# Kernel tuning notes

Measured on AMD Instinct MI355X. Metric: run time of the kernel, lower is better.

## Reference

```python
import jax, jax.numpy as jnp
import numpy as np

B, T, W = 8, 4096, 1024          # batch, byte seq len, words per sequence
DB, DW = 64, 512                 # byte_embed_dim, word_embed_dim
NH = 2                           # highway layers per block
VOCAB = 264                      # 256 bytes + 4 + 4 specials
BPE_MARK, WORD_MARK = 4, 3       # bpe_mask_idx, word_mask_idx


def _make_seg_ids():
    # ragged word lengths in {3,4,5}, mean 4, summing to T per sequence
    rng = np.random.default_rng(0)
    seg = np.empty((B, T), np.int32)
    base = T // W
    for b in range(B):
        delta = np.zeros(W, np.int64)
        q = W // 4
        idx = rng.permutation(W)
        delta[idx[:q]] = 1
        delta[idx[q:2 * q]] = -1
        seg[b] = np.repeat(np.arange(W), base + delta)
    return jnp.asarray(seg)


def setup_inputs() -> dict:
    key = jax.random.key(0)
    ks = jax.random.split(key, 12)
    s = 0.05
    byte_tokens = jax.random.randint(ks[0], (B, T), 4, VOCAB)
    bpe_mask = jax.random.bernoulli(ks[1], 0.25, (B, T))
    word_mask = jax.random.bernoulli(ks[2], 0.05, (B, T))
    seg_ids = _make_seg_ids()
    tok_emb = (jax.random.normal(ks[3], (VOCAB, DB)) * s).at[0].set(0.0)  # padding_idx=0 row zeroed
    inp = {
        'byte_tokens': byte_tokens, 'bpe_mask': bpe_mask, 'word_mask': word_mask,
        'seg_ids': seg_ids, 'tok_emb': tok_emb,
        'conv0_w': jax.random.normal(ks[4], (3, DB, DW)) * s, 'conv0_b': jnp.zeros((DW,)),
        'hw0_wg': jax.random.normal(ks[5], (NH, DW, DW)) * s, 'hw0_bg': jnp.zeros((NH, DW)),
        'hw0_wh': jax.random.normal(ks[6], (NH, DW, DW)) * s, 'hw0_bh': jnp.zeros((NH, DW)),
        'conv1_w': jax.random.normal(ks[7], (3, DW, DW)) * s, 'conv1_b': jnp.zeros((DW,)),
        'hw1_wg': jax.random.normal(ks[8], (NH, DW, DW)) * s, 'hw1_bg': jnp.zeros((NH, DW)),
        'hw1_wh': jax.random.normal(ks[9], (NH, DW, DW)) * s, 'hw1_bh': jnp.zeros((NH, DW)),
        'proj_w': jax.random.normal(ks[10], (DW, DW)) * s, 'proj_b': jnp.zeros((DW,)),
    }
    return inp


def _conv_highway(x, cw, cb, wg, bg, wh, bh, residual):
    # 1D same-padded conv over sequence, optional residual, relu, then highways
    y = jax.lax.conv_general_dilated(x, cw, (1,), 'SAME',
                                     dimension_numbers=('NWC', 'WIO', 'NWC')) + cb
    if residual:
        y = y + x
    y = jax.nn.relu(y)
    for i in range(NH):
        g = jax.nn.sigmoid(y @ wg[i] + bg[i])
        h = jax.nn.relu(y @ wh[i] + bh[i])
        y = g * h + (1.0 - g) * y
    return y


def reference(byte_tokens, bpe_mask, word_mask, seg_ids, tok_emb,
              conv0_w, conv0_b, hw0_wg, hw0_bg, hw0_wh, hw0_bh,
              conv1_w, conv1_b, hw1_wg, hw1_bg, hw1_wh, hw1_bh,
              proj_w, proj_b):
    # byte embedding + marker embeddings (pad idx 0 -> zero row)
    x = (tok_emb[byte_tokens]
         + tok_emb[jnp.where(bpe_mask, BPE_MARK, 0)]
         + tok_emb[jnp.where(word_mask, WORD_MARK, 0)])          # [B,T,DB]
    x = _conv_highway(x, conv0_w, conv0_b, hw0_wg, hw0_bg, hw0_wh, hw0_bh, False)
    x = _conv_highway(x, conv1_w, conv1_b, hw1_wg, hw1_bg, hw1_wh, hw1_bh, True)
    # ragged per-word segment max over bytes (fused, replaces python loops)
    seg_max = jax.vmap(lambda xi, si: jax.ops.segment_max(xi, si, num_segments=W))
    x = seg_max(x, seg_ids)                                       # [B,W,DW]
    return x @ proj_w + proj_b
```

## Files before the change

### kernel.cpp

```cpp
#include <hip/hip_runtime.h>
#include <hip/hip_bf16.h>

using bf16 = __hip_bfloat16;
typedef __attribute__((ext_vector_type(8))) short s8v;
typedef __attribute__((ext_vector_type(4))) float f4v;

#define T_SEQ 4096
#define DWC 512

__device__ __forceinline__ float fin(float v) {
    return (v == v && fabsf(v) < 1e30f) ? v : 0.0f;
}
__device__ __forceinline__ float ldf(const void* p, size_t i, int f32) {
    return f32 ? ((const float*)p)[i] : __bfloat162float(((const bf16*)p)[i]);
}
__device__ __forceinline__ float b2f(short s) {
    unsigned u = ((unsigned)(unsigned short)s) << 16;
    return __builtin_bit_cast(float, u);
}
__device__ __forceinline__ short f2b(float v) {
    bf16 b = __float2bfloat16(v);
    return __builtin_bit_cast(short, b);
}
__device__ __forceinline__ uint4 ld16(const short* p) { return *(const uint4*)p; }

__device__ __forceinline__ void swz(int L, int G, int& bx, int& by) {
    int k8 = L & 7, sl = L >> 3;
    int gp = G >> 5;
    bx = sl & 3;
    by = k8 * gp + (sl >> 2);
}

__device__ __forceinline__ int swidx(int row, int ch) {
    return row * 32 + ((ch ^ ((row >> 1) & 3)) << 3);
}

__global__ __launch_bounds__(256) void diag_kernel(bf16* __restrict__ out, int n, float v)
{
    int i = blockIdx.x * 256 + threadIdx.x;
    if (i < n) out[i] = __float2bfloat16(i == 0 ? v : 0.0f);
}

__global__ __launch_bounds__(256) void detect_kernel(
    const int* __restrict__ tok, const unsigned char* __restrict__ bpe,
    const unsigned char* __restrict__ wm, const int* __restrict__ seg,
    const unsigned int* __restrict__ embw, int* __restrict__ flags)
{
    __shared__ int sh[5];
    int tid = threadIdx.x;
    if (tid < 5) sh[tid] = 0;
    __syncthreads();
    int bo = 0, bm = 0, wo = 0, wmid = 0;
    for (int i = tid; i < 16384; i += 256) {
        int odd = 2 * i + 1;
        if (bpe[odd]) bo = 1;
        if (wm[odd])  wo = 1;
        int mid = 8 * (i & 4095) + 4;
        if (bpe[mid]) bm = 1;
        if (wm[mid])  wmid = 1;
    }
    if (bo)   atomicOr(&sh[0], 1);
    if (bm)   atomicOr(&sh[1], 1);
    if (wo)   atomicOr(&sh[2], 1);
    if (wmid) atomicOr(&sh[3], 1);
    if (tid < 32 && embw[32 + tid] != 0u) atomicOr(&sh[4], 1);
    __syncthreads();
    if (tid == 0) {
        flags[0] = (tok[32767] != 0) ? 0 : 1;
        flags[1] = sh[0] ? 1 : (sh[1] ? 4 : 8);
        flags[2] = sh[2] ? 1 : (sh[3] ? 4 : 8);
        flags[3] = (seg[32767] != 0) ? 0 : 1;
        flags[4] = sh[4] ? 0 : 1;
    }
}

#define WB_TOTAL 3249664
#define EMB4_ELEMS (264 * 4 * 64)
__global__ __launch_bounds__(256) void convert_weights(
    const void* c0w, const void* c0b, const void* h0g, const void* h0bg,
    const void* h0h, const void* h0bh, const void* c1w, const void* c1b,
    const void* h1g, const void* h1bg, const void* h1h, const void* h1bh,
    const void* pw, const void* pb, const void* emb,
    const int* __restrict__ flags, short* __restrict__ WB)
{
    int f32 = flags[4];
    size_t i = (size_t)blockIdx.x * 256 + threadIdx.x;
    if (i >= WB_TOTAL + EMB4_ELEMS) return;
    if (i >= WB_TOTAL) {
        size_t o = i - WB_TOTAL;
        size_t t = o >> 8, v = (o >> 6) & 3, c = o & 63;
        float val = ldf(emb, t * 64 + c, f32);
        if (v & 1) val += ldf(emb, 4 * 64 + c, f32);
        if (v & 2) val += ldf(emb, 3 * 64 + c, f32);
        WB[i] = f2b(fin(val));
        return;
    }
    const void* src; size_t si;
    if (i < 98304)        { size_t n = i / 192, k = i % 192; src = c0w; si = k * 512 + n; }
    else if (i < 98816)   { src = c0b;  si = i - 98304; }
    else if (i < 623104)  { size_t o = i - 98816;  size_t l = o >> 18; o &= 262143;
                            size_t n = o >> 9, k = o & 511; src = h0g; si = (l << 18) + k * 512 + n; }
    else if (i < 624128)  { src = h0bg; si = i - 623104; }
    else if (i < 1148416) { size_t o = i - 624128; size_t l = o >> 18; o &= 262143;
                            size_t n = o >> 9, k = o & 511; src = h0h; si = (l << 18) + k * 512 + n; }
    else if (i < 1149440) { src = h0bh; si = i - 1148416; }
    else if (i < 1935872) { size_t o = i - 1149440; size_t n = o / 1536, k = o % 1536;
                            src = c1w; si = k * 512 + n; }
    else if (i < 1936384) { src = c1b;  si = i - 1935872; }
    else if (i < 2460672) { size_t o = i - 1936384; size_t l = o >> 18; o &= 262143;
                            size_t n = o >> 9, k = o & 511; src = h1g; si = (l << 18) + k * 512 + n; }
    else if (i < 2461696) { src = h1bg; si = i - 2460672; }
    else if (i < 2985984) { size_t o = i - 2461696; size_t l = o >> 18; o &= 262143;
                            size_t n = o >> 9, k = o & 511; src = h1h; si = (l << 18) + k * 512 + n; }
    else if (i < 2987008) { src = h1bh; si = i - 2985984; }
    else if (i < 3249152) { size_t o = i - 2987008; size_t n = o >> 9, k = o & 511;
                            src = pw; si = k * 512 + n; }
    else                  { src = pb;   si = i - 3249152; }
    WB[i] = f2b(ldf(src, si, f32));
}

__global__ __launch_bounds__(512) void conv0_mfma(
    const int* __restrict__ tok, const unsigned char* __restrict__ bpe,
    const unsigned char* __restrict__ wm, const short* __restrict__ emb4,
    const int* __restrict__ flags, const short* __restrict__ WT,
    const short* __restrict__ bias, short* __restrict__ Out)
{
    constexpr int K = 192;
    constexpr int NIT = 3;
    __shared__ __align__(16) short As[2][256 * 32];
    __shared__ __align__(16) short Bs[2][256 * 32];
    int bx, by;
    swz(blockIdx.x, gridDim.x, bx, by);
    const int bm = by * 128, bn = bx * 128;
    const int tid = threadIdx.x;
    const int wave = tid >> 6, lane = tid & 63;
    const int wmr = (wave >> 1) * 32, wnc = (wave & 1) * 64;
    const int q = lane >> 4, ln16 = lane & 15;
    const int sr = tid >> 2, sch = tid & 3;
    const int tt = (bm + sr) & (T_SEQ - 1);
    const int is64t = flags[0];
    const int wb = flags[1], ww = flags[2];
    const short* Bb = WT + (size_t)(bn + sr) * K + sch * 8;

    f4v acc[2][4] = {};
    uint4 rA0, rA1, rB0, rB1;
    const uint4 z4 = make_uint4(0, 0, 0, 0);

    auto loadA = [&](int tap, uint4& a0, uint4& a1) {
        int ts = tt + tap - 1;
        if ((unsigned)ts < (unsigned)T_SEQ) {
            int bt = bm + sr + tap - 1;
            int tk = is64t ? (int)((const long long*)tok)[bt] : tok[bt];
            tk = min(max(tk, 0), 263);
            int v = (bpe[(size_t)bt * wb] ? 1 : 0) | (wm[(size_t)bt * ww] ? 2 : 0);
            const short* row = emb4 + ((size_t)tk * 4 + v) * 64;
            a0 = ld16(row + sch * 8);
            a1 = ld16(row + 32 + sch * 8);
        } else { a0 = z4; a1 = z4; }
    };

    loadA(0, rA0, rA1);
    rB0 = ld16(Bb);
    rB1 = ld16(Bb + 32);
    *(uint4*)(&As[0][swidx(sr, sch)])       = rA0;
    *(uint4*)(&As[0][swidx(128 + sr, sch)]) = rA1;
    *(uint4*)(&Bs[0][swidx(sr, sch)])       = rB0;
    *(uint4*)(&Bs[0][swidx(128 + sr, sch)]) = rB1;
    __syncthreads();
    int p = 0;

    for (int it = 0; it < NIT; ++it) {
        const bool more = (it + 1 < NIT);
        if (more) {
            int kn = (it + 1) * 64;
            loadA(it + 1, rA0, rA1);
            rB0 = ld16(Bb + kn);
            rB1 = ld16(Bb + kn + 32);
        }
        #pragma unroll
        for (int ks = 0; ks < 2; ks++) {
            s8v af[2], bf[4];
            #pragma unroll
            for (int mi = 0; mi < 2; mi++)
                af[mi] = *(const s8v*)(&As[p][swidx(128 * ks + wmr + mi * 16 + ln16, q)]);
            #pragma unroll
            for (int ni = 0; ni < 4; ni++)
                bf[ni] = *(const s8v*)(&Bs[p][swidx(128 * ks + wnc + ni * 16 + ln16, q)]);
            #pragma unroll
            for (int mi = 0; mi < 2; mi++)
                #pragma unroll
                for (int ni = 0; ni < 4; ni++)
                    acc[mi][ni] = __builtin_amdgcn_mfma_f32_16x16x32_bf16(
                        af[mi], bf[ni], acc[mi][ni], 0, 0, 0);
        }
        if (more) {
            *(uint4*)(&As[p ^ 1][swidx(sr, sch)])       = rA0;
            *(uint4*)(&As[p ^ 1][swidx(128 + sr, sch)]) = rA1;
            *(uint4*)(&Bs[p ^ 1][swidx(sr, sch)])       = rB0;
            *(uint4*)(&Bs[p ^ 1][swidx(128 + sr, sch)]) = rB1;
            __syncthreads();
            p ^= 1;
        }
    }

    #pragma unroll
    for (int mi = 0; mi < 2; mi++)
        #pragma unroll
        for (int ni = 0; ni < 4; ni++) {
            int col = bn + wnc + ni * 16 + ln16;
            float bv = b2f(bias[col]);
            #pragma unroll
            for (int r = 0; r < 4; r++) {
                int orow = bm + wmr + mi * 16 + q * 4 + r;
                Out[(size_t)orow * DWC + col] =
                    f2b(fin(fmaxf(acc[mi][ni][r] + bv, 0.0f)));
            }
        }
}

__global__ __launch_bounds__(512) void conv1_mfma(
    const short* __restrict__ A, const short* __restrict__ WT,
    const short* __restrict__ bias, short* __restrict__ Out)
{
    constexpr int IC = 512;
    constexpr int K = 3 * IC;
    constexpr int NIT = K / 64;
    __shared__ __align__(16) short As[2][256 * 32];
    __shared__ __align__(16) short Bs[2][256 * 32];
    int bx, by;
    swz(blockIdx.x, gridDim.x, bx, by);
    const int bm = by * 128, bn = bx * 128;
    const int tid = threadIdx.x;
    const int wave = tid >> 6, lane = tid & 63;
    const int wmr = (wave >> 1) * 32, wnc = (wave & 1) * 64;
    const int q = lane >> 4, ln16 = lane & 15;
    const int sr = tid >> 2, sch = tid & 3;
    const int tt = (bm + sr) & (T_SEQ - 1);
    const short* Bb = WT + (size_t)(bn + sr) * K + sch * 8;

    f4v acc[2][4] = {};
    uint4 rA0, rA1, rB0, rB1;
    const uint4 z4 = make_uint4(0, 0, 0, 0);

    {
        int ts = tt - 1;
        bool ok = (ts >= 0 && ts < T_SEQ);
        const short* sa = A + (size_t)(bm + sr - 1) * IC + sch * 8;
        rA0 = ok ? ld16(sa) : z4;
        rA1 = ok ? ld16(sa + 32) : z4;
        rB0 = ld16(Bb);
        rB1 = ld16(Bb + 32);
    }
    *(uint4*)(&As[0][swidx(sr, sch)])       = rA0;
    *(uint4*)(&As[0][swidx(128 + sr, sch)]) = rA1;
    *(uint4*)(&Bs[0][swidx(sr, sch)])       = rB0;
    *(uint4*)(&Bs[0][swidx(128 + sr, sch)]) = rB1;
    __syncthreads();
    int p = 0;

    for (int it = 0; it < NIT; ++it) {
        const bool more = (it + 1 < NIT);
        if (more) {
            int kn = (it + 1) * 64;
            int tap = kn / IC, c0 = kn - tap * IC;
            int ts = tt + tap - 1;
            bool ok = (ts >= 0 && ts < T_SEQ);
            const short* sa = A + (size_t)(bm + sr + tap - 1) * IC + c0 + sch * 8;
            rA0 = ok ? ld16(sa) : z4;
            rA1 = ok ? ld16(sa + 32) : z4;
            rB0 = ld16(Bb + kn);
            rB1 = ld16(Bb + kn + 32);
        }
        #pragma unroll
        for (int ks = 0; ks < 2; ks++) {
            s8v af[2], bf[4];
            #pragma unroll
            for (int mi = 0; mi < 2; mi++)
                af[mi] = *(const s8v*)(&As[p][swidx(128 * ks + wmr + mi * 16 + ln16, q)]);
            #pragma unroll
            for (int ni = 0; ni < 4; ni++)
                bf[ni] = *(const s8v*)(&Bs[p][swidx(128 * ks + wnc + ni * 16 + ln16, q)]);
            #pragma unroll
            for (int mi = 0; mi < 2; mi++)
                #pragma unroll
                for (int ni = 0; ni < 4; ni++)
                    acc[mi][ni] = __builtin_amdgcn_mfma_f32_16x16x32_bf16(
                        af[mi], bf[ni], acc[mi][ni], 0, 0, 0);
        }
        if (more) {
            *(uint4*)(&As[p ^ 1][swidx(sr, sch)])       = rA0;
            *(uint4*)(&As[p ^ 1][swidx(128 + sr, sch)]) = rA1;
            *(uint4*)(&Bs[p ^ 1][swidx(sr, sch)])       = rB0;
            *(uint4*)(&Bs[p ^ 1][swidx(128 + sr, sch)]) = rB1;
            __syncthreads();
            p ^= 1;
        }
    }

    #pragma unroll
    for (int mi = 0; mi < 2; mi++)
        #pragma unroll
        for (int ni = 0; ni < 4; ni++) {
            int col = bn + wnc + ni * 16 + ln16;
            float bv = b2f(bias[col]);
            #pragma unroll
            for (int r = 0; r < 4; r++) {
                int orow = bm + wmr + mi * 16 + q * 4 + r;
                float v = acc[mi][ni][r] + bv + b2f(A[(size_t)orow * IC + col]);
                Out[(size_t)orow * DWC + col] = f2b(fin(fmaxf(v, 0.0f)));
            }
        }
}

__global__ __launch_bounds__(512) void highway_mfma8(
    const short* __restrict__ Y, const short* __restrict__ WgT,
    const short* __restrict__ bg, const short* __restrict__ WhT,
    const short* __restrict__ bh, short* __restrict__ Out)
{
    constexpr int IC = DWC;
    constexpr int NIT = IC / 64;
    __shared__ __align__(16) short As [2][512 * 32];
    __shared__ __align__(16) short Bgs[2][256 * 32];
    __shared__ __align__(16) short Bhs[2][256 * 32];
    int bx, by;
    swz(blockIdx.x, gridDim.x, bx, by);
    const int bm = by * 256, bn = bx * 128;
    const int tid = threadIdx.x;
    const int wave = tid >> 6, lane = tid & 63;
    const int wmr = (wave >> 2) * 128;
    const int wnc = (wave & 3) * 32;
    const int q = lane >> 4, ln16 = lane & 15;
    const int sr = tid >> 2, sch = tid & 3;

    const short* A0 = Y   + (size_t)(bm + sr) * IC + sch * 8;
    const short* A1 = A0 + 128 * IC;
    const short* G0 = WgT + (size_t)(bn + sr) * IC + sch * 8;
    const short* H0 = WhT + (size_t)(bn + sr) * IC + sch * 8;

    f4v accg[8][2] = {};
    f4v acch[8][2] = {};
    uint4 rA0, rA1, rA2, rA3, rG0, rG1, rH0, rH1;

    rA0 = ld16(A0);      rA1 = ld16(A0 + 32);
    rA2 = ld16(A1);      rA3 = ld16(A1 + 32);
    rG0 = ld16(G0);      rG1 = ld16(G0 + 32);
    rH0 = ld16(H0);      rH1 = ld16(H0 + 32);
    *(uint4*)(&As [0][swidx(      sr, sch)]) = rA0;
    *(uint4*)(&As [0][swidx(256 + sr, sch)]) = rA1;
    *(uint4*)(&As [0][swidx(128 + sr, sch)]) = rA2;
    *(uint4*)(&As [0][swidx(384 + sr, sch)]) = rA3;
    *(uint4*)(&Bgs[0][swidx(      sr, sch)]) = rG0;
    *(uint4*)(&Bgs[0][swidx(128 + sr, sch)]) = rG1;
    *(uint4*)(&Bhs[0][swidx(      sr, sch)]) = rH0;
    *(uint4*)(&Bhs[0][swidx(128 + sr, sch)]) = rH1;
    __syncthreads();
    int p = 0;

    for (int it = 0; it < NIT; ++it) {
        const bool more = (it + 1 < NIT);
        const int kn = (it + 1) * 64;
        const short* Ap = &As [p][0];
        const short* Gp = &Bgs[p][0];
        const short* Hp = &Bhs[p][0];

        s8v af[4][2], bgf[2][2];
        #pragma unroll
        for (int mi = 0; mi < 4; mi++)
            #pragma unroll
            for (int ks = 0; ks < 2; ks++)
                af[mi][ks] = *(const s8v*)(&Ap[swidx(ks * 256 + wmr + mi * 16 + ln16, q)]);
        #pragma unroll
        for (int ni = 0; ni < 2; ni++)
            #pragma unroll
            for (int ks = 0; ks < 2; ks++)
                bgf[ni][ks] = *(const s8v*)(&Gp[swidx(ks * 128 + wnc + ni * 16 + ln16, q)]);
        if (more) {
            rA0 = ld16(A0 + kn); rA1 = ld16(A0 + kn + 32);
            rA2 = ld16(A1 + kn); rA3 = ld16(A1 + kn + 32);
        }
        __builtin_amdgcn_s_barrier();
        __builtin_amdgcn_s_setprio(1);
        #pragma unroll
        for (int mi = 0; mi < 4; mi++)
            #pragma unroll
            for (int ni = 0; ni < 2; ni++)
                #pragma unroll
                for (int ks = 0; ks < 2; ks++)
                    accg[mi][ni] = __builtin_amdgcn_mfma_f32_16x16x32_bf16(
                        af[mi][ks], bgf[ni][ks], accg[mi][ni], 0, 0, 0);
        __builtin_amdgcn_s_setprio(0);
        __builtin_amdgcn_s_barrier();

        s8v bhf[2][2];
        #pragma unroll
        for (int ni = 0; ni < 2; ni++)
            #pragma unroll
            for (int ks = 0; ks < 2; ks++)
                bhf[ni][ks] = *(const s8v*)(&Hp[swidx(ks * 128 + wnc + ni * 16 + ln16, q)]);
        if (more) { rG0 = ld16(G0 + kn); rG1 = ld16(G0 + kn + 32); }
        __builtin_amdgcn_s_barrier();
        __builtin_amdgcn_s_setprio(1);
        #pragma unroll
        for (int mi = 0; mi < 4; mi++)
            #pragma unroll
            for (int ni = 0; ni < 2; ni++)
                #pragma unroll
                for (int ks = 0; ks < 2; ks++)
                    acch[mi][ni] = __builtin_amdgcn_mfma_f32_16x16x32_bf16(
                        af[mi][ks], bhf[ni][ks], acch[mi][ni], 0, 0, 0);
        __builtin_amdgcn_s_setprio(0);
        __builtin_amdgcn_s_barrier();

        #pragma unroll
        for (int mi = 0; mi < 4; mi++)
            #pragma unroll
            for (int ks = 0; ks < 2; ks++)
                af[mi][ks] = *(const s8v*)(&Ap[swidx(ks * 256 + wmr + 64 + mi * 16 + ln16, q)]);
        if (more) { rH0 = ld16(H0 + kn); rH1 = ld16(H0 + kn + 32); }
        __builtin_amdgcn_s_barrier();
        __builtin_amdgcn_s_setprio(1);
        #pragma unroll
        for (int mi = 0; mi < 4; mi++)
            #pragma unroll
            for (int ni = 0; ni < 2; ni++)
                #pragma unroll
                for (int ks = 0; ks < 2; ks++)
                    accg[4 + mi][ni] = __builtin_amdgcn_mfma_f32_16x16x32_bf16(
                        af[mi][ks], bgf[ni][ks], accg[4 + mi][ni], 0, 0, 0);
        __builtin_amdgcn_s_setprio(0);
        __builtin_amdgcn_s_barrier();

        __builtin_amdgcn_s_setprio(1);
        #pragma unroll
        for (int mi = 0; mi < 4; mi++)
            #pragma unroll
            for (int ni = 0; ni < 2; ni++)
                #pragma unroll
                for (int ks = 0; ks < 2; ks++)
                    acch[4 + mi][ni] = __builtin_amdgcn_mfma_f32_16x16x32_bf16(
                        af[mi][ks], bhf[ni][ks], acch[4 + mi][ni], 0, 0, 0);
        __builtin_amdgcn_s_setprio(0);
        __builtin_amdgcn_sched_barrier(0);
        if (more) {
            short* An = &As [p ^ 1][0];
            short* Gn = &Bgs[p ^ 1][0];
            short* Hn = &Bhs[p ^ 1][0];
            *(uint4*)(&An[swidx(      sr, sch)]) = rA0;
            *(uint4*)(&An[swidx(256 + sr, sch)]) = rA1;
            *(uint4*)(&An[swidx(128 + sr, sch)]) = rA2;
            *(uint4*)(&An[swidx(384 + sr, sch)]) = rA3;
            *(uint4*)(&Gn[swidx(      sr, sch)]) = rG0;
            *(uint4*)(&Gn[swidx(128 + sr, sch)]) = rG1;
            *(uint4*)(&Hn[swidx(      sr, sch)]) = rH0;
            *(uint4*)(&Hn[swidx(128 + sr, sch)]) = rH1;
            asm volatile("s_waitcnt lgkmcnt(0)" ::: "memory");
            __builtin_amdgcn_s_barrier();
            p ^= 1;
        }
    }

    #pragma unroll
    for (int mi = 0; mi < 8; mi++)
        #pragma unroll
        for (int ni = 0; ni < 2; ni++) {
            int col = bn + wnc + ni * 16 + ln16;
            float bgv = b2f(bg[col]);
            float bhv = b2f(bh[col]);
            #pragma unroll
            for (int r = 0; r < 4; r++) {
                int orow = bm + wmr + mi * 16 + q * 4 + r;
                float g = 1.0f / (1.0f + expf(-(accg[mi][ni][r] + bgv)));
                float h = fmaxf(acch[mi][ni][r] + bhv, 0.0f);
                float yv = b2f(Y[(size_t)orow * DWC + col]);
                Out[(size_t)orow * DWC + col] = f2b(fin(g * h + (1.0f - g) * yv));
            }
        }
}

__global__ __launch_bounds__(512) void proj_mfma(
    const short* __restrict__ A, const short* __restrict__ WT,
    const short* __restrict__ bias, const int* __restrict__ flags,
    void* __restrict__ Out, int oroff)
{
    __shared__ __align__(16) short As[128 * 32];
    __shared__ __align__(16) short Bs[128 * 32];
    int bx, by;
    swz(blockIdx.x, gridDim.x, bx, by);
    const int bm = by * 128, bn = bx * 128;
    const int tid = threadIdx.x;
    const int wave = tid >> 6, lane = tid & 63;
    const int wmr = (wave >> 1) * 32, wnc = (wave & 1) * 64;
    const int q = lane >> 4, ln16 = lane & 15;
    const int sr = tid >> 2, sch = tid & 3;
    const int sw = swidx(sr, sch);
    const int f32 = flags[4];
    const short* A0 = A  + (size_t)(bm + sr) * DWC + sch * 8;
    const short* B0 = WT + (size_t)(bn + sr) * DWC + sch * 8;

    f4v acc[2][4] = {};
    uint4 rA = ld16(A0), rB = ld16(B0);

    for (int k0 = 0; k0 < DWC; k0 += 32) {
        *(uint4*)(&As[sw]) = rA;
        *(uint4*)(&Bs[sw]) = rB;
        __syncthreads();
        if (k0 + 32 < DWC) {
            int kn = k0 + 32;
            rA = ld16(A0 + kn); rB = ld16(B0 + kn);
        }
        s8v af[2], bf[4];
        #pragma unroll
        for (int mi = 0; mi < 2; mi++) af[mi] = *(const s8v*)(&As[swidx(wmr + mi * 16 + ln16, q)]);
        #pragma unroll
        for (int ni = 0; ni < 4; ni++) bf[ni] = *(const s8v*)(&Bs[swidx(wnc + ni * 16 + ln16, q)]);
        #pragma unroll
        for (int mi = 0; mi < 2; mi++)
            #pragma unroll
            for (int ni = 0; ni < 4; ni++)
                acc[mi][ni] = __builtin_amdgcn_mfma_f32_16x16x32_bf16(
                    af[mi], bf[ni], acc[mi][ni], 0, 0, 0);
        __syncthreads();
    }

    #pragma unroll
    for (int mi = 0; mi < 2; mi++)
        #pragma unroll
        for (int ni = 0; ni < 4; ni++) {
            int col = bn + wnc + ni * 16 + ln16;
            float bv = b2f(bias[col]);
            #pragma unroll
            for (int r = 0; r < 4; r++) {
                int orow = bm + wmr + mi * 16 + q * 4 + r;
                float v = fin(acc[mi][ni][r] + bv);
                size_t oi = (size_t)(oroff + orow) * DWC + col;
                if (f32) ((float*)Out)[oi] = v;
                else     ((bf16*)Out)[oi] = __float2bfloat16(v);
            }
        }
}

__global__ __launch_bounds__(256) void bounds_kernel(
    const int* __restrict__ seg, const int* __restrict__ flags,
    int* __restrict__ wstart, int* __restrict__ wend, int bt0)
{
    int il = blockIdx.x * 256 + threadIdx.x;
    int ig = bt0 + il;
    int is64 = flags[3];
    const long long* seg64 = (const long long*)seg;
    int t = il & (T_SEQ - 1);
    int bl = il >> 12;
    int s  = (is64 ? (int)seg64[ig] : seg[ig]) & 1023;
    int sp = (t == 0)         ? -1 : ((is64 ? (int)seg64[ig - 1] : seg[ig - 1]) & 1023);
    int sn = (t == T_SEQ - 1) ? -1 : ((is64 ? (int)seg64[ig + 1] : seg[ig + 1]) & 1023);
    int bw = (bl << 10) + s;
    if (sp != s) wstart[bw] = t;
    if (sn != s) wend[bw] = t;
}

__global__ __launch_bounds__(512) void segmax_kernel(
    const short* __restrict__ Y, const int* __restrict__ wstart,
    const int* __restrict__ wend, short* __restrict__ Out)
{
    int bw = blockIdx.x;
    int d = threadIdx.x;
    int bl = bw >> 10;
    int s = wstart[bw], e = wend[bw];
    s = min(max(s, 0), T_SEQ - 1);
    e = min(max(e, s), T_SEQ - 1);
    float m = b2f(Y[(size_t)((bl << 12) + s) * DWC + d]);
    for (int t = s + 1; t <= e; ++t)
        m = fmaxf(m, b2f(Y[(size_t)((bl << 12) + t) * DWC + d]));
    Out[(size_t)bw * DWC + d] = f2b(fin(m));
}

extern "C" void kernel_launch(void* const* d_in, const int* in_sizes, int n_in,
                              void* d_out, int out_size, void* d_ws, size_t ws_size,
                              hipStream_t stream)
{
    static const int expect[19] = {32768, 32768, 32768, 32768, 16896,
                                   98304, 512, 524288, 1024, 524288, 1024,
                                   786432, 512, 524288, 1024, 524288, 1024,
                                   262144, 512};
    int bad = -1;
    if (n_in < 19) bad = 31;
    else for (int i = 0; i < 19; i++) if (in_sizes[i] != expect[i]) { bad = i; break; }
    if (bad >= 0) {
        diag_kernel<<<dim3((out_size + 255) / 256), dim3(256), 0, stream>>>(
            (bf16*)d_out, out_size, 1e35f * (float)(1 + bad));
        return;
    }

    char* ws = (char*)d_ws;
    const size_t WBREG = 8ull << 20;
    short* WB    = (short*)ws;
    int*   flags = (int*)(ws + (7u << 20));
    const size_t perC = 8388608 + 8192 + 64;
    int C = 8;
    while (C > 1 && WBREG + (size_t)C * perC > ws_size) C >>= 1;
    if (WBREG + (size_t)C * perC > ws_size) {
        float ws_mib = (float)((double)ws_size / 1048576.0);
        diag_kernel<<<dim3((out_size + 255) / 256), dim3(256), 0, stream>>>(
            (bf16*)d_out, out_size, 1e30f * (16.0f + ws_mib));
        return;
    }

    const int*  byte_tokens = (const int*)d_in[0];
    const unsigned char* bpe_mask = (const unsigned char*)d_in[1];
    const unsigned char* word_mask = (const unsigned char*)d_in[2];
    const int*  seg_ids     = (const int*)d_in[3];
    const void* tok_emb = d_in[4];

    detect_kernel<<<dim3(1), dim3(256), 0, stream>>>(
        byte_tokens, bpe_mask, word_mask, seg_ids,
        (const unsigned int*)tok_emb, flags);

    convert_weights<<<dim3((WB_TOTAL + EMB4_ELEMS + 255) / 256), dim3(256), 0, stream>>>(
        d_in[5], d_in[6], d_in[7], d_in[8], d_in[9], d_in[10],
        d_in[11], d_in[12], d_in[13], d_in[14], d_in[15], d_in[16],
        d_in[17], d_in[18], tok_emb, flags, WB);

    short* c0wT = WB;            short* c0b  = WB + 98304;
    short* h0gT = WB + 98816;    short* h0bg = WB + 623104;
    short* h0hT = WB + 624128;   short* h0bh = WB + 1148416;
    short* c1wT = WB + 1149440;  short* c1b  = WB + 1935872;
    short* h1gT = WB + 1936384;  short* h1bg = WB + 2460672;
    short* h1hT = WB + 2461696;  short* h1bh = WB + 2985984;
    short* pwT  = WB + 2987008;  short* pb   = WB + 3249152;
    short* emb4 = WB + WB_TOTAL;
    const int LOFF = 262144, LBOFF = 512;

    for (int b0 = 0; b0 < 8; b0 += C) {
        const int rows  = C * T_SEQ;
        const int words = C * 1024;
        char*  chunk  = ws + WBREG;
        short* U      = (short*)chunk;
        short* V      = (short*)(chunk + (size_t)C * 4194304);
        int*   wstart = (int*)(chunk + (size_t)C * 8388608);
        int*   wend   = wstart + words;
        short* segout = U;

        dim3 gg(4 * (rows / 128));
        dim3 gh(4 * (rows / 256));
        conv0_mfma<<<gg, dim3(512), 0, stream>>>(
            byte_tokens + (size_t)b0 * T_SEQ,
            bpe_mask, word_mask, emb4, flags, c0wT, c0b, U);

        highway_mfma8<<<gh, dim3(512), 0, stream>>>(U, h0gT, h0bg, h0hT, h0bh, V);
        highway_mfma8<<<gh, dim3(512), 0, stream>>>(V, h0gT + LOFF, h0bg + LBOFF,
                                                    h0hT + LOFF, h0bh + LBOFF, U);

        conv1_mfma<<<gg, dim3(512), 0, stream>>>(U, c1wT, c1b, V);

        highway_mfma8<<<gh, dim3(512), 0, stream>>>(V, h1gT, h1bg, h1hT, h1bh, U);
        highway_mfma8<<<gh, dim3(512), 0, stream>>>(U, h1gT + LOFF, h1bg + LBOFF,
                                                    h1hT + LOFF, h1bh + LBOFF, V);

        bounds_kernel<<<dim3(rows / 256), dim3(256), 0, stream>>>(
            seg_ids, flags, wstart, wend, b0 * T_SEQ);

        segmax_kernel<<<dim3(words), dim3(512), 0, stream>>>(V, wstart, wend, segout);

        proj_mfma<<<dim3(4 * (words / 128)), dim3(512), 0, stream>>>(
            segout, pwT, pb, flags, d_out, b0 * 1024);
    }
}
```

Measured before the change: 429.4 us.

## Enlarge conv1 tile to 256x256 with staged ping-pong MFMA schedule

Rewrites the conv1 GEMM kernel to compute 256x256 output tiles per 512-thread block instead of 128x128. Each wave now accumulates a 128x64 sub-tile, and the per-iteration work is split into four MFMA phases, with global prefetch loads interleaved between phases and s_setprio raised around the MFMA bursts. Block indices are remapped so that each XCD gets contiguous row tiles. The goal is more data reuse per LDS load and better overlap of memory with MFMA, at the cost of doubled LDS use (128 KB), far more accumulator registers, and fewer blocks in the grid.

```diff
diff --git a/kernel.cpp b/kernel.cpp
--- a/kernel.cpp
+++ b/kernel.cpp
@@ -218,87 +218,157 @@
         }
 }
 
-__global__ __launch_bounds__(512) void conv1_mfma(
+__global__ __launch_bounds__(512) void conv1_mfma256(
     const short* __restrict__ A, const short* __restrict__ WT,
     const short* __restrict__ bias, short* __restrict__ Out)
 {
     constexpr int IC = 512;
     constexpr int K = 3 * IC;
     constexpr int NIT = K / 64;
-    __shared__ __align__(16) short As[2][256 * 32];
-    __shared__ __align__(16) short Bs[2][256 * 32];
-    int bx, by;
-    swz(blockIdx.x, gridDim.x, bx, by);
-    const int bm = by * 128, bn = bx * 128;
+    __shared__ __align__(16) short As[2][512 * 32];
+    __shared__ __align__(16) short Bs[2][512 * 32];
+    {
+    }
+    const int L = blockIdx.x, G = gridDim.x;
+    const int xcd = L & 7, sl = L >> 3, mt = G >> 4;
+    const int bx = sl & 1, by = xcd * mt + (sl >> 1);
+    const int bm = by * 256, bn = bx * 256;
     const int tid = threadIdx.x;
     const int wave = tid >> 6, lane = tid & 63;
-    const int wmr = (wave >> 1) * 32, wnc = (wave & 1) * 64;
+    const int wmr = (wave >> 2) * 128;
+    const int wnc = (wave & 3) * 64;
     const int q = lane >> 4, ln16 = lane & 15;
     const int sr = tid >> 2, sch = tid & 3;
     const int tt = (bm + sr) & (T_SEQ - 1);
-    const short* Bb = WT + (size_t)(bn + sr) * K + sch * 8;
-
-    f4v acc[2][4] = {};
-    uint4 rA0, rA1, rB0, rB1;
+
+    const short* Bb  = WT + (size_t)(bn + sr) * K + sch * 8;
+    const short* Bb2 = Bb + (size_t)128 * K;
+
+    f4v acc[8][4] = {};
+    uint4 rA0, rA1, rA2, rA3, rB0, rB1, rB2, rB3;
     const uint4 z4 = make_uint4(0, 0, 0, 0);
 
-    {
-        int ts = tt - 1;
-        bool ok = (ts >= 0 && ts < T_SEQ);
-        const short* sa = A + (size_t)(bm + sr - 1) * IC + sch * 8;
-        rA0 = ok ? ld16(sa) : z4;
-        rA1 = ok ? ld16(sa + 32) : z4;
-        rB0 = ld16(Bb);
-        rB1 = ld16(Bb + 32);
-    }
-    *(uint4*)(&As[0][swidx(sr, sch)])       = rA0;
-    *(uint4*)(&As[0][swidx(128 + sr, sch)]) = rA1;
-    *(uint4*)(&Bs[0][swidx(sr, sch)])       = rB0;
-    *(uint4*)(&Bs[0][swidx(128 + sr, sch)]) = rB1;
+    auto loadA = [&](int kn) {
+        int tap = kn >> 9, c0 = kn & 511;
+        int ts = tt + tap - 1;
+        bool ok1 = ((unsigned)ts < (unsigned)T_SEQ);
+        bool ok2 = ((unsigned)(ts + 128) < (unsigned)T_SEQ);
+        const short* sa = A + (size_t)(bm + sr + tap - 1) * IC + c0 + sch * 8;
+        rA0 = ok1 ? ld16(sa) : z4;
+        rA1 = ok1 ? ld16(sa + 32) : z4;
+        rA2 = ok2 ? ld16(sa + 128 * IC) : z4;
+        rA3 = ok2 ? ld16(sa + 128 * IC + 32) : z4;
+    };
+    auto loadB = [&](int kn) {
+        rB0 = ld16(Bb + kn);  rB1 = ld16(Bb + kn + 32);
+        rB2 = ld16(Bb2 + kn); rB3 = ld16(Bb2 + kn + 32);
+    };
+    auto publish = [&](int pp) {
+        *(uint4*)(&As[pp][swidx(      sr, sch)]) = rA0;
+        *(uint4*)(&As[pp][swidx(256 + sr, sch)]) = rA1;
+        *(uint4*)(&As[pp][swidx(128 + sr, sch)]) = rA2;
+        *(uint4*)(&As[pp][swidx(384 + sr, sch)]) = rA3;
+        *(uint4*)(&Bs[pp][swidx(      sr, sch)]) = rB0;
+        *(uint4*)(&Bs[pp][swidx(256 + sr, sch)]) = rB1;
+        *(uint4*)(&Bs[pp][swidx(128 + sr, sch)]) = rB2;
+        *(uint4*)(&Bs[pp][swidx(384 + sr, sch)]) = rB3;
+    };
+
+    loadA(0);
+    loadB(0);
+    publish(0);
     __syncthreads();
     int p = 0;
 
     for (int it = 0; it < NIT; ++it) {
         const bool more = (it + 1 < NIT);
+        const int kn = (it + 1) * 64;
+        const short* Ap = &As[p][0];
+        const short* Bp = &Bs[p][0];
+        s8v af[4][2], bfL[2][2], bfH[2][2];
+
+        #pragma unroll
+        for (int mi = 0; mi < 4; mi++)
+            #pragma unroll
+            for (int ks = 0; ks < 2; ks++)
+                af[mi][ks] = *(const s8v*)(&Ap[swidx(ks * 256 + wmr + mi * 16 + ln16, q)]);
+        #pragma unroll
+        for (int ni = 0; ni < 2; ni++)
+            #pragma unroll
+            for (int ks = 0; ks < 2; ks++)
+                bfL[ni][ks] = *(const s8v*)(&Bp[swidx(ks * 256 + wnc + ni * 16 + ln16, q)]);
+        if (more) loadA(kn);
+        __builtin_amdgcn_s_barrier();
+        __builtin_amdgcn_s_setprio(1);
+        #pragma unroll
+        for (int mi = 0; mi < 4; mi++)
+            #pragma unroll
+            for (int ni = 0; ni < 2; ni++)
+                #pragma unroll
+                for (int ks = 0; ks < 2; ks++)
+                    acc[mi][ni] = __builtin_amdgcn_mfma_f32_16x16x32_bf16(
+                        af[mi][ks], bfL[ni][ks], acc[mi][ni], 0, 0, 0);
+        __builtin_amdgcn_s_setprio(0);
+        __builtin_amdgcn_s_barrier();
+
+        #pragma unroll
+        for (int ni = 0; ni < 2; ni++)
+            #pragma unroll
+            for (int ks = 0; ks < 2; ks++)
+                bfH[ni][ks] = *(const s8v*)(&Bp[swidx(ks * 256 + wnc + 32 + ni * 16 + ln16, q)]);
+        if (more) loadB(kn);
+        __builtin_amdgcn_s_barrier();
+        __builtin_amdgcn_s_setprio(1);
+        #pragma unroll
+        for (int mi = 0; mi < 4; mi++)
+            #pragma unroll
+            for (int ni = 0; ni < 2; ni++)
+                #pragma unroll
+                for (int ks = 0; ks < 2; ks++)
+                    acc[mi][2 + ni] = __builtin_amdgcn_mfma_f32_16x16x32_bf16(
+                        af[mi][ks], bfH[ni][ks], acc[mi][2 + ni], 0, 0, 0);
+        __builtin_amdgcn_s_setprio(0);
+        __builtin_amdgcn_s_barrier();
+
+        #pragma unroll
+        for (int mi = 0; mi < 4; mi++)
+            #pragma unroll
+            for (int ks = 0; ks < 2; ks++)
+                af[mi][ks] = *(const s8v*)(&Ap[swidx(ks * 256 + wmr + 64 + mi * 16 + ln16, q)]);
+        __builtin_amdgcn_s_barrier();
+        __builtin_amdgcn_s_setprio(1);
+        #pragma unroll
+        for (int mi = 0; mi < 4; mi++)
+            #pragma unroll
+            for (int ni = 0; ni < 2; ni++)
+                #pragma unroll
+                for (int ks = 0; ks < 2; ks++)
+                    acc[4 + mi][2 + ni] = __builtin_amdgcn_mfma_f32_16x16x32_bf16(
+                        af[mi][ks], bfH[ni][ks], acc[4 + mi][2 + ni], 0, 0, 0);
+        __builtin_amdgcn_s_setprio(0);
+        __builtin_amdgcn_s_barrier();
+
+        __builtin_amdgcn_s_setprio(1);
+        #pragma unroll
+        for (int mi = 0; mi < 4; mi++)
+            #pragma unroll
+            for (int ni = 0; ni < 2; ni++)
+                #pragma unroll
+                for (int ks = 0; ks < 2; ks++)
+                    acc[4 + mi][ni] = __builtin_amdgcn_mfma_f32_16x16x32_bf16(
+                        af[mi][ks], bfL[ni][ks], acc[4 + mi][ni], 0, 0, 0);
+        __builtin_amdgcn_s_setprio(0);
+        __builtin_amdgcn_sched_barrier(0);
         if (more) {
-            int kn = (it + 1) * 64;
-            int tap = kn / IC, c0 = kn - tap * IC;
-            int ts = tt + tap - 1;
-            bool ok = (ts >= 0 && ts < T_SEQ);
-            const short* sa = A + (size_t)(bm + sr + tap - 1) * IC + c0 + sch * 8;
-            rA0 = ok ? ld16(sa) : z4;
-            rA1 = ok ? ld16(sa + 32) : z4;
-            rB0 = ld16(Bb + kn);
-            rB1 = ld16(Bb + kn + 32);
-        }
-        #pragma unroll
-        for (int ks = 0; ks < 2; ks++) {
-            s8v af[2], bf[4];
-            #pragma unroll
-            for (int mi = 0; mi < 2; mi++)
-                af[mi] = *(const s8v*)(&As[p][swidx(128 * ks + wmr + mi * 16 + ln16, q)]);
-            #pragma unroll
-            for (int ni = 0; ni < 4; ni++)
-                bf[ni] = *(const s8v*)(&Bs[p][swidx(128 * ks + wnc + ni * 16 + ln16, q)]);
-            #pragma unroll
-            for (int mi = 0; mi < 2; mi++)
-                #pragma unroll
-                for (int ni = 0; ni < 4; ni++)
-                    acc[mi][ni] = __builtin_amdgcn_mfma_f32_16x16x32_bf16(
-                        af[mi], bf[ni], acc[mi][ni], 0, 0, 0);
-        }
-        if (more) {
-            *(uint4*)(&As[p ^ 1][swidx(sr, sch)])       = rA0;
-            *(uint4*)(&As[p ^ 1][swidx(128 + sr, sch)]) = rA1;
-            *(uint4*)(&Bs[p ^ 1][swidx(sr, sch)])       = rB0;
-            *(uint4*)(&Bs[p ^ 1][swidx(128 + sr, sch)]) = rB1;
-            __syncthreads();
+            publish(p ^ 1);
+            asm volatile("s_waitcnt lgkmcnt(0)" ::: "memory");
+            __builtin_amdgcn_s_barrier();
             p ^= 1;
         }
     }
 
     #pragma unroll
-    for (int mi = 0; mi < 2; mi++)
+    for (int mi = 0; mi < 8; mi++)
         #pragma unroll
         for (int ni = 0; ni < 4; ni++) {
             int col = bn + wnc + ni * 16 + ln16;
@@ -641,6 +711,7 @@
 
         dim3 gg(4 * (rows / 128));
         dim3 gh(4 * (rows / 256));
+        dim3 gc1(2 * (rows / 256));
         conv0_mfma<<<gg, dim3(512), 0, stream>>>(
             byte_tokens + (size_t)b0 * T_SEQ,
             bpe_mask, word_mask, emb4, flags, c0wT, c0b, U);
@@ -649,7 +720,7 @@
         highway_mfma8<<<gh, dim3(512), 0, stream>>>(V, h0gT + LOFF, h0bg + LBOFF,
                                                     h0hT + LOFF, h0bh + LBOFF, U);
 
-        conv1_mfma<<<gg, dim3(512), 0, stream>>>(U, c1wT, c1b, V);
+        conv1_mfma256<<<gc1, dim3(512), 0, stream>>>(U, c1wT, c1b, V);
 
         highway_mfma8<<<gh, dim3(512), 0, stream>>>(V, h1gT, h1bg, h1hT, h1bh, U);
         highway_mfma8<<<gh, dim3(512), 0, stream>>>(U, h1gT + LOFF, h1bg + LBOFF,
```

Measured after the change: 434.9 us. About the same (+1.3%).

## Stage highway GEMM tiles via direct global-to-LDS loads

Applied to the files above, without the earlier changes.

Replaces the register-staged global loads and later LDS stores in the highway MFMA kernel with global_load_lds instructions that write straight into the swizzled shared-memory buffers. The aim is to free VGPRs and drop the separate ds_write phase at the end of each k-iteration, so the double-buffered pipeline overlaps better. The per-lane address mapping is rearranged so each wave's contiguous 1KB LDS segment matches the existing XOR swizzle, which adds risk if that mapping or the vmcnt synchronisation is wrong.

```diff
diff --git a/kernel.cpp b/kernel.cpp
--- a/kernel.cpp
+++ b/kernel.cpp
@@ -23,6 +23,12 @@
     return __builtin_bit_cast(short, b);
 }
 __device__ __forceinline__ uint4 ld16(const short* p) { return *(const uint4*)p; }
+
+__device__ __forceinline__ void gl_lds16(const short* g, short* l) {
+    __builtin_amdgcn_global_load_lds(
+        (const __attribute__((address_space(1))) void*)g,
+        (__attribute__((address_space(3))) void*)l, 16, 0, 0);
+}
 
 __device__ __forceinline__ void swz(int L, int G, int& bx, int& by) {
     int k8 = L & 7, sl = L >> 3;
@@ -330,29 +336,41 @@
     const int wmr = (wave >> 2) * 128;
     const int wnc = (wave & 3) * 32;
     const int q = lane >> 4, ln16 = lane & 15;
-    const int sr = tid >> 2, sch = tid & 3;
-
-    const short* A0 = Y   + (size_t)(bm + sr) * IC + sch * 8;
-    const short* A1 = A0 + 128 * IC;
-    const short* G0 = WgT + (size_t)(bn + sr) * IC + sch * 8;
-    const short* H0 = WhT + (size_t)(bn + sr) * IC + sch * 8;
+
+    const int rr = (wave << 4) + (lane >> 2);
+    const int ch = (lane & 3) ^ ((rr >> 1) & 3);
+    const short* gA[4]; const short* gG[2]; const short* gH[2];
+    #pragma unroll
+    for (int j = 0; j < 4; j++)
+        gA[j] = Y + (size_t)(bm + ((j & 1) << 7) + rr) * IC + (j >> 1) * 32 + ch * 8;
+    #pragma unroll
+    for (int j = 0; j < 2; j++) {
+        gG[j] = WgT + (size_t)(bn + rr) * IC + j * 32 + ch * 8;
+        gH[j] = WhT + (size_t)(bn + rr) * IC + j * 32 + ch * 8;
+    }
+    const int wb1k = wave << 10;
 
     f4v accg[8][2] = {};
     f4v acch[8][2] = {};
-    uint4 rA0, rA1, rA2, rA3, rG0, rG1, rH0, rH1;
-
-    rA0 = ld16(A0);      rA1 = ld16(A0 + 32);
-    rA2 = ld16(A1);      rA3 = ld16(A1 + 32);
-    rG0 = ld16(G0);      rG1 = ld16(G0 + 32);
-    rH0 = ld16(H0);      rH1 = ld16(H0 + 32);
-    *(uint4*)(&As [0][swidx(      sr, sch)]) = rA0;
-    *(uint4*)(&As [0][swidx(256 + sr, sch)]) = rA1;
-    *(uint4*)(&As [0][swidx(128 + sr, sch)]) = rA2;
-    *(uint4*)(&As [0][swidx(384 + sr, sch)]) = rA3;
-    *(uint4*)(&Bgs[0][swidx(      sr, sch)]) = rG0;
-    *(uint4*)(&Bgs[0][swidx(128 + sr, sch)]) = rG1;
-    *(uint4*)(&Bhs[0][swidx(      sr, sch)]) = rH0;
-    *(uint4*)(&Bhs[0][swidx(128 + sr, sch)]) = rH1;
+
+    auto stageA = [&](int pp, int kk) {
+        char* b = (char*)&As[pp][0] + wb1k;
+        #pragma unroll
+        for (int j = 0; j < 4; j++) gl_lds16(gA[j] + kk, (short*)(b + (j << 13)));
+    };
+    auto stageG = [&](int pp, int kk) {
+        char* b = (char*)&Bgs[pp][0] + wb1k;
+        #pragma unroll
+        for (int j = 0; j < 2; j++) gl_lds16(gG[j] + kk, (short*)(b + (j << 13)));
+    };
+    auto stageH = [&](int pp, int kk) {
+        char* b = (char*)&Bhs[pp][0] + wb1k;
+        #pragma unroll
+        for (int j = 0; j < 2; j++) gl_lds16(gH[j] + kk, (short*)(b + (j << 13)));
+    };
+
+    stageA(0, 0); stageG(0, 0); stageH(0, 0);
+    asm volatile("s_waitcnt vmcnt(0)" ::: "memory");
     __syncthreads();
     int p = 0;
 
@@ -374,10 +392,7 @@
             #pragma unroll
             for (int ks = 0; ks < 2; ks++)
                 bgf[ni][ks] = *(const s8v*)(&Gp[swidx(ks * 128 + wnc + ni * 16 + ln16, q)]);
-        if (more) {
-            rA0 = ld16(A0 + kn); rA1 = ld16(A0 + kn + 32);
-            rA2 = ld16(A1 + kn); rA3 = ld16(A1 + kn + 32);
-        }
+        if (more) stageA(p ^ 1, kn);
         __builtin_amdgcn_s_barrier();
         __builtin_amdgcn_s_setprio(1);
         #pragma unroll
@@ -397,7 +412,7 @@
             #pragma unroll
             for (int ks = 0; ks < 2; ks++)
                 bhf[ni][ks] = *(const s8v*)(&Hp[swidx(ks * 128 + wnc + ni * 16 + ln16, q)]);
-        if (more) { rG0 = ld16(G0 + kn); rG1 = ld16(G0 + kn + 32); }
+        if (more) stageG(p ^ 1, kn);
         __builtin_amdgcn_s_barrier();
         __builtin_amdgcn_s_setprio(1);
         #pragma unroll
@@ -416,7 +431,7 @@
             #pragma unroll
             for (int ks = 0; ks < 2; ks++)
                 af[mi][ks] = *(const s8v*)(&Ap[swidx(ks * 256 + wmr + 64 + mi * 16 + ln16, q)]);
-        if (more) { rH0 = ld16(H0 + kn); rH1 = ld16(H0 + kn + 32); }
+        if (more) stageH(p ^ 1, kn);
         __builtin_amdgcn_s_barrier();
         __builtin_amdgcn_s_setprio(1);
         #pragma unroll
@@ -440,20 +455,8 @@
                     acch[4 + mi][ni] = __builtin_amdgcn_mfma_f32_16x16x32_bf16(
                         af[mi][ks], bhf[ni][ks], acch[4 + mi][ni], 0, 0, 0);
         __builtin_amdgcn_s_setprio(0);
-        __builtin_amdgcn_sched_barrier(0);
         if (more) {
-            short* An = &As [p ^ 1][0];
-            short* Gn = &Bgs[p ^ 1][0];
-            short* Hn = &Bhs[p ^ 1][0];
-            *(uint4*)(&An[swidx(      sr, sch)]) = rA0;
-            *(uint4*)(&An[swidx(256 + sr, sch)]) = rA1;
-            *(uint4*)(&An[swidx(128 + sr, sch)]) = rA2;
-            *(uint4*)(&An[swidx(384 + sr, sch)]) = rA3;
-            *(uint4*)(&Gn[swidx(      sr, sch)]) = rG0;
-            *(uint4*)(&Gn[swidx(128 + sr, sch)]) = rG1;
-            *(uint4*)(&Hn[swidx(      sr, sch)]) = rH0;
-            *(uint4*)(&Hn[swidx(128 + sr, sch)]) = rH1;
-            asm volatile("s_waitcnt lgkmcnt(0)" ::: "memory");
+            asm volatile("s_waitcnt vmcnt(0)" ::: "memory");
             __builtin_amdgcn_s_barrier();
             p ^= 1;
         }
```

After: 419.0 us. -2.4%, faster.
